# Kernel optimization log

Measured on AMD Instinct MI355X. Metric: run time of the kernel, lower is better.

Reference implementation:

```python
import jax, jax.numpy as jnp
import numpy as np

HIDDEN = 2048
NUM_HEADS = 16
HEAD = HIDDEN // NUM_HEADS  # 128
B, S = 4, 2048  # equal-length prefill sequences (cu_seqlens = arange(B+1)*S)


def setup_inputs() -> dict:
    key = jax.random.key(0)
    ks = jax.random.split(key, 5)
    return {
        "hidden_states": jax.random.normal(ks[0], (B * S, HIDDEN), jnp.float32),
        # fused QKV weight: rows ordered [q(all heads), k(all heads), v(all heads)]
        "w_qkv": jax.random.normal(ks[1], (3 * HIDDEN, HIDDEN), jnp.float32) * 0.02,
        "b_qkv": jax.random.normal(ks[2], (3 * HIDDEN,), jnp.float32) * 0.02,
        "w_dense": jax.random.normal(ks[3], (HIDDEN, HIDDEN), jnp.float32) * 0.02,
        "b_dense": jax.random.normal(ks[4], (HIDDEN,), jnp.float32) * 0.02,
        "batch_size": B,
        "seq_len": S,
    }


def reference(hidden_states, w_qkv, b_qkv, w_dense, b_dense, batch_size, seq_len):
    # QKV projection: [T, hidden] -> [T, 3, H, D]
    qkv = hidden_states @ w_qkv.T + b_qkv
    qkv = qkv.reshape(batch_size, seq_len, 3, NUM_HEADS, HEAD)
    q, k, v = qkv[:, :, 0], qkv[:, :, 1], qkv[:, :, 2]  # each [B, S, H, D]

    softmax_scale = HEAD ** -0.5
    # varlen causal flash attention (prefill path), per-sequence causal mask
    scores = jnp.einsum("bqhd,bkhd->bhqk", q, k) * softmax_scale
    causal = jnp.tril(jnp.ones((seq_len, seq_len), dtype=bool))
    scores = jnp.where(causal, scores, jnp.finfo(scores.dtype).min)
    probs = jax.nn.softmax(scores, axis=-1)
    attn = jnp.einsum("bhqk,bkhd->bqhd", probs, v)  # [B, S, H, D]

    attn = attn.reshape(batch_size * seq_len, NUM_HEADS * HEAD)
    # output projection (resid dropout p=0 -> identity)
    return attn @ w_dense.T + b_dense
```

## Files before the change

### kernel.cpp

```cpp
#include <hip/hip_runtime.h>
#include <hip/hip_bf16.h>

#define HIDDEN 2048
#define NHEADS 16
#define HEADD  128
#define BATCH  4
#define SEQ    2048
#define MROWS  (BATCH*SEQ)
#define NQKV   (3*HIDDEN)

typedef __attribute__((ext_vector_type(8))) short bf16x8;
typedef __attribute__((ext_vector_type(4))) float f32x4;

__device__ inline unsigned short f2bf(float f) {
  unsigned int u = __builtin_bit_cast(unsigned int, f);
  u += 0x7FFF + ((u >> 16) & 1);
  return (unsigned short)(u >> 16);
}

__device__ inline void async16(const void* g, void* s) {
  __builtin_amdgcn_global_load_lds(
      (__attribute__((address_space(1))) void*)(g),
      (__attribute__((address_space(3))) void*)(s), 16, 0, 0);
}

#define PH_BAR() asm volatile("s_barrier" ::: "memory")
#define LGKM0()  asm volatile("s_waitcnt lgkmcnt(0)" ::: "memory")
#define VMC6()   asm volatile("s_waitcnt vmcnt(6)" ::: "memory")
#define VMC0()   asm volatile("s_waitcnt vmcnt(0)" ::: "memory")

__global__ __launch_bounds__(256)
void cvt_f32_bf16(const float* __restrict__ in, unsigned short* __restrict__ out, int n) {
  int i = (blockIdx.x * 256 + threadIdx.x) * 8;
  if (i + 8 <= n) {
    float4 a = *(const float4*)&in[i];
    float4 b = *(const float4*)&in[i + 4];
    unsigned short o[8];
    o[0] = f2bf(a.x); o[1] = f2bf(a.y); o[2] = f2bf(a.z); o[3] = f2bf(a.w);
    o[4] = f2bf(b.x); o[5] = f2bf(b.y); o[6] = f2bf(b.z); o[7] = f2bf(b.w);
    *(uint4*)&out[i] = *(uint4*)o;
  }
}

#define MFMA_QUAD(AB, NB, AF, BF)                                           \
  _Pragma("unroll")                                                         \
  for (int mi = 0; mi < 4; ++mi)                                            \
    _Pragma("unroll")                                                       \
    for (int e = 0; e < 2; ++e)                                             \
      _Pragma("unroll")                                                     \
      for (int ks = 0; ks < 2; ++ks)                                        \
        acc[(AB) + mi][(NB) + e] = __builtin_amdgcn_mfma_f32_16x16x32_bf16( \
            AF[mi][ks], BF[e][ks], acc[(AB) + mi][(NB) + e], 0, 0, 0);

#define RD_A(DST, BUF, H)                                                   \
  _Pragma("unroll")                                                         \
  for (int mi = 0; mi < 4; ++mi) {                                          \
    DST[mi][0] = rdA(BUF, H, mi, 0);                                        \
    DST[mi][1] = rdA(BUF, H, mi, 1);                                        \
  }

#define RD_B(DST, BUF, H)                                                   \
  _Pragma("unroll")                                                         \
  for (int e = 0; e < 2; ++e) {                                             \
    DST[e][0] = rdB(BUF, H, e, 0);                                          \
    DST[e][1] = rdB(BUF, H, e, 1);                                          \
  }

template<int OUT_BF16>
__global__ __launch_bounds__(512, 2)
void gemm256(const unsigned short* __restrict__ A,
             const unsigned short* __restrict__ Bw,
             const float* __restrict__ bias,
             void* __restrict__ Cout, int M, int N, int K) {
  __shared__ __align__(16) unsigned short L[2][2][2][8192];

  const int t = threadIdx.x;
  const int lane = t & 63, wv = t >> 6;
  const int r = lane & 15, q = lane >> 4;
  const int wm = wv >> 2, wn = wv & 3;
  const int r7 = r & 7;

  const int gx = gridDim.x;
  const int nwg = gx * (int)gridDim.y;
  const int id = (int)blockIdx.y * gx + (int)blockIdx.x;
  const int swz = (id & 7) * (nwg >> 3) + (id >> 3);
  const int m0 = (swz / gx) * 256;
  const int n0 = (swz % gx) * 256;

  const int sub = t >> 3;
  const int cb = (t & 7) ^ (sub & 7);
  unsigned offA[2][2], offB[2][2];
#pragma unroll
  for (int ld = 0; ld < 2; ++ld) {
    int row = ld * 64 + sub;
    int fs = row >> 4, r16 = row & 15;
    int gA = (fs & 3) | ((fs >> 2) << 3);
    int gB = (fs & 1) | ((fs >> 1) << 2);
#pragma unroll
    for (int h = 0; h < 2; ++h) {
      offA[h][ld] = (unsigned)(m0 + (gA | (h << 2)) * 16 + r16) * (unsigned)K + cb * 8;
      offB[h][ld] = (unsigned)(n0 + (gB | (h << 1)) * 16 + r16) * (unsigned)K + cb * 8;
    }
  }

  auto stgA = [&](int buf, int h, int tile) {
    async16(A + (size_t)(offA[h][0] + (unsigned)tile * 64), &L[buf][0][h][t * 8]);
    async16(A + (size_t)(offA[h][1] + (unsigned)tile * 64), &L[buf][0][h][4096 + t * 8]);
  };
  auto stgB = [&](int buf, int h, int tile) {
    async16(Bw + (size_t)(offB[h][0] + (unsigned)tile * 64), &L[buf][1][h][t * 8]);
    async16(Bw + (size_t)(offB[h][1] + (unsigned)tile * 64), &L[buf][1][h][4096 + t * 8]);
  };
  auto rdA = [&](int buf, int h, int mi, int ks) -> bf16x8 {
    int row = (wm * 4 + mi) * 16 + r;
    int c = (ks * 4 + q) ^ r7;
    return *(const bf16x8*)&L[buf][0][h][row * 64 + c * 8];
  };
  auto rdB = [&](int buf, int h, int e, int ks) -> bf16x8 {
    int row = (wn * 2 + e) * 16 + r;
    int c = (ks * 4 + q) ^ r7;
    return *(const bf16x8*)&L[buf][1][h][row * 64 + c * 8];
  };

  f32x4 acc[8][4] = {};
  bf16x8 a0[4][2], a1[4][2], b0[2][2], b1[2][2];

  stgA(0, 0, 0); stgB(0, 0, 0); stgA(0, 1, 0); stgB(0, 1, 0);
  stgA(1, 0, 1); stgB(1, 0, 1); stgA(1, 1, 1);
  VMC6(); PH_BAR();

  const int NT = K >> 6;
  const int NITER = K >> 7;
#pragma unroll 1
  for (int i = 0; i < NITER; ++i) {
    const int ta = 2 * i + 1;
    int tb = 2 * i + 2; if (tb > NT - 1) tb = NT - 1;
    int tc = 2 * i + 3; if (tc > NT - 1) tc = NT - 1;

    RD_A(a0, 0, 0); RD_B(b0, 0, 0);
    stgB(1, 1, ta);
    PH_BAR(); LGKM0(); __builtin_amdgcn_s_setprio(1);
    MFMA_QUAD(0, 0, a0, b0);
    __builtin_amdgcn_s_setprio(0); PH_BAR();

    RD_A(a1, 0, 1);
    stgA(0, 0, tb);
    PH_BAR(); LGKM0(); __builtin_amdgcn_s_setprio(1);
    MFMA_QUAD(4, 0, a1, b0);
    __builtin_amdgcn_s_setprio(0); PH_BAR();

    RD_B(b1, 0, 1);
    stgB(0, 0, tb);
    PH_BAR(); LGKM0(); __builtin_amdgcn_s_setprio(1);
    MFMA_QUAD(4, 2, a1, b1);
    __builtin_amdgcn_s_setprio(0); PH_BAR();

    stgA(0, 1, tb);
    PH_BAR(); LGKM0(); __builtin_amdgcn_s_setprio(1);
    MFMA_QUAD(0, 2, a0, b1);
    __builtin_amdgcn_s_setprio(0); VMC6(); PH_BAR();

    RD_A(a0, 1, 0); RD_B(b0, 1, 0);
    stgB(0, 1, tb);
    PH_BAR(); LGKM0(); __builtin_amdgcn_s_setprio(1);
    MFMA_QUAD(0, 0, a0, b0);
    __builtin_amdgcn_s_setprio(0); PH_BAR();

    RD_A(a1, 1, 1);
    stgA(1, 0, tc);
    PH_BAR(); LGKM0(); __builtin_amdgcn_s_setprio(1);
    MFMA_QUAD(4, 0, a1, b0);
    __builtin_amdgcn_s_setprio(0); PH_BAR();

    RD_B(b1, 1, 1);
    stgB(1, 0, tc);
    PH_BAR(); LGKM0(); __builtin_amdgcn_s_setprio(1);
    MFMA_QUAD(4, 2, a1, b1);
    __builtin_amdgcn_s_setprio(0); PH_BAR();

    stgA(1, 1, tc);
    PH_BAR(); LGKM0(); __builtin_amdgcn_s_setprio(1);
    MFMA_QUAD(0, 2, a0, b1);
    __builtin_amdgcn_s_setprio(0); VMC6(); PH_BAR();
  }
  VMC0();

  float bv[4];
#pragma unroll
  for (int ni = 0; ni < 4; ++ni) bv[ni] = bias[n0 + (wn * 4 + ni) * 16 + r];
#pragma unroll
  for (int ai = 0; ai < 8; ++ai) {
    int grow = m0 + (wm * 8 + ai) * 16 + q * 4;
#pragma unroll
    for (int ni = 0; ni < 4; ++ni) {
      int gcol = n0 + (wn * 4 + ni) * 16 + r;
#pragma unroll
      for (int rr = 0; rr < 4; ++rr) {
        float v = acc[ai][ni][rr] + bv[ni];
        if (OUT_BF16)
          ((unsigned short*)Cout)[(size_t)(grow + rr) * N + gcol] = f2bf(v);
        else
          ((float*)Cout)[(size_t)(grow + rr) * N + gcol] = v;
      }
    }
  }
}

__global__ __launch_bounds__(256, 2)
void flash_attn(const unsigned short* __restrict__ qkv,
                unsigned short* __restrict__ attn,
                float* __restrict__ outP,
                float* __restrict__ lsumB)
{
  __shared__ __align__(16) unsigned short Ks[64][128];
  __shared__ __align__(16) unsigned short Vt[128][64];

  const int t = threadIdx.x;
  const int lane = t & 63, wv = t >> 6;
  const int r = lane & 15, q = lane >> 4;
  const int b = blockIdx.y >> 4, h = blockIdx.y & 15;

  int f = (int)blockIdx.x, qt, c;
  if (f < 8)       { qt = 15 - f; c = 0; }
  else if (f < 16) { qt = 23 - f; c = 1; }
  else             { qt = 23 - f; c = 0; }
  const int q0 = qt * 128;
  const int t0 = c * 16;
  int t1 = 2 * qt + 2; if (t1 > t0 + 16) t1 = t0 + 16;

  unsigned short* Ps = &Ks[0][0] + wv * 2048;

  const size_t rs = NQKV;
  const unsigned short* qbase = qkv + (size_t)(b * SEQ) * rs + h * HEADD;
  const unsigned short* kbase = qbase + HIDDEN;
  const unsigned short* vbase = qbase + 2 * HIDDEN;

  bf16x8 qf[2][4];
  for (int i = 0; i < 2; ++i)
    for (int ks = 0; ks < 4; ++ks)
      qf[i][ks] = *(const bf16x8*)(qbase +
          (size_t)(q0 + wv * 32 + i * 16 + r) * rs + ks * 32 + q * 8);

  f32x4 accO[2][8] = {};
  float lsum[2][4] = {};

  const int diag0 = 2 * qt;
  const float sc2 = 0.08838834764831845f * 1.4426950408889634f;

  const int koct = t & 15, krb = t >> 4;
  const int bd4 = t & 15, bkv4 = t >> 4;

  uint4 kreg[4], vreg[4];
  for (int s = 0; s < 4; ++s)
    kreg[s] = *(const uint4*)(kbase + (size_t)(t0 * 64 + krb + 16 * s) * rs + koct * 8);
  for (int jr = 0; jr < 4; ++jr)
    vreg[jr] = *(const uint4*)(vbase + (size_t)(t0 * 64 + bkv4 * 4 + jr) * rs + bd4 * 8);

  for (int tk = t0; tk < t1; ++tk) {
    LGKM0(); PH_BAR();
    for (int s = 0; s < 4; ++s) {
      int row = krb + 16 * s;
      int cbk = koct ^ (row & 7);
      *(uint4*)&Ks[row][cbk * 8] = kreg[s];
    }
    for (int jj = 0; jj < 8; ++jj) {
      int d = bd4 * 8 + jj;
      int cbk = (bkv4 >> 1) ^ jj ^ (bd4 & 7);
      unsigned short tmp[4];
      for (int jr = 0; jr < 4; ++jr)
        tmp[jr] = ((const unsigned short*)&vreg[jr])[jj];
      *(uint2*)&Vt[d][cbk * 8 + (bkv4 & 1) * 4] = *(const uint2*)tmp;
    }
    LGKM0(); PH_BAR();
    if (tk + 1 < t1) {
      for (int s = 0; s < 4; ++s)
        kreg[s] = *(const uint4*)(kbase + (size_t)((tk + 1) * 64 + krb + 16 * s) * rs + koct * 8);
      for (int jr = 0; jr < 4; ++jr)
        vreg[jr] = *(const uint4*)(vbase + (size_t)((tk + 1) * 64 + bkv4 * 4 + jr) * rs + bd4 * 8);
    }

    f32x4 s[2][4] = {};
    __builtin_amdgcn_s_setprio(1);
    for (int ks = 0; ks < 4; ++ks) {
      bf16x8 bk[4];
      for (int j = 0; j < 4; ++j) {
        int row = j * 16 + r;
        int cbk = (ks * 4 + q) ^ (r & 7);
        bk[j] = *(const bf16x8*)&Ks[row][cbk * 8];
      }
      for (int i = 0; i < 2; ++i)
        for (int j = 0; j < 4; ++j)
          s[i][j] = __builtin_amdgcn_mfma_f32_16x16x32_bf16(qf[i][ks], bk[j], s[i][j], 0, 0, 0);
    }
    __builtin_amdgcn_s_setprio(0);
    LGKM0(); PH_BAR();

    const bool diag = (tk >= diag0);
    for (int i = 0; i < 2; ++i) {
      float pvv[4][4];
      for (int j = 0; j < 4; ++j)
        for (int rr = 0; rr < 4; ++rr) {
          float v = s[i][j][rr] * sc2;
          if (diag) {
            int kvp = tk * 64 + j * 16 + r;
            int qp = q0 + wv * 32 + i * 16 + q * 4 + rr;
            if (kvp > qp) v = -1e30f;
          }
          float p = __builtin_amdgcn_exp2f(v);
          pvv[j][rr] = p;
          lsum[i][rr] += p;
        }
      for (int j = 0; j < 4; ++j)
        for (int rr = 0; rr < 4; ++rr) {
          int m = i * 16 + q * 4 + rr;
          int k = j * 16 + r;
          int cbk = (k >> 3) ^ (m & 7);
          Ps[m * 64 + cbk * 8 + (k & 7)] = f2bf(pvv[j][rr]);
        }
    }

    __builtin_amdgcn_s_setprio(1);
    for (int ks2 = 0; ks2 < 2; ++ks2) {
      bf16x8 ap[2];
      for (int i = 0; i < 2; ++i) {
        int m = i * 16 + r;
        int cbk = (ks2 * 4 + q) ^ (r & 7);
        ap[i] = *(const bf16x8*)&Ps[m * 64 + cbk * 8];
      }
      for (int n = 0; n < 8; ++n) {
        int dd = n * 16 + r;
        int cbk = (ks2 * 4 + q) ^ (r & 7) ^ ((n * 2 + (r >> 3)) & 7);
        bf16x8 bvv = *(const bf16x8*)&Vt[dd][cbk * 8];
        for (int i = 0; i < 2; ++i)
          accO[i][n] = __builtin_amdgcn_mfma_f32_16x16x32_bf16(ap[i], bvv, accO[i][n], 0, 0, 0);
      }
    }
    __builtin_amdgcn_s_setprio(0);
  }

  for (int i = 0; i < 2; ++i)
    for (int rr = 0; rr < 4; ++rr) {
      float l = lsum[i][rr];
      for (int off = 1; off < 16; off <<= 1)
        l += __shfl_xor(l, off, 64);
      lsum[i][rr] = l;
    }

  if (qt < 8) {
    for (int i = 0; i < 2; ++i)
      for (int rr = 0; rr < 4; ++rr) {
        int row = q0 + wv * 32 + i * 16 + q * 4 + rr;
        float inv = 1.0f / lsum[i][rr];
        size_t obase = (size_t)(b * SEQ + row) * HIDDEN + h * HEADD;
        for (int n = 0; n < 8; ++n)
          attn[obase + n * 16 + r] = f2bf(accO[i][n][rr] * inv);
      }
  } else {
    const int cb4 = c * 4 + b;
    for (int i = 0; i < 2; ++i)
      for (int rr = 0; rr < 4; ++rr) {
        int row = q0 + wv * 32 + i * 16 + q * 4 + rr;
        int rl = row - 1024;
        if (r == 0)
          lsumB[(size_t)(cb4 * 1024 + rl) * 16 + h] = lsum[i][rr];
        size_t obase = (size_t)(cb4 * 1024 + rl) * 2048 + h * HEADD;
        for (int n = 0; n < 8; ++n)
          outP[obase + n * 16 + r] = accO[i][n][rr];
      }
  }
}

__global__ __launch_bounds__(256)
void attn_norm(const float* __restrict__ outP, const float* __restrict__ lsumB,
               unsigned short* __restrict__ attn) {
  size_t j = ((size_t)blockIdx.x * 256 + threadIdx.x) * 8;
  int b = (int)(j >> 21);
  int rl = (int)(j >> 11) & 1023;
  int col = (int)j & 2047;
  int h = col >> 7;
  float l = lsumB[(size_t)(b * 1024 + rl) * 16 + h]
          + lsumB[(size_t)((4 + b) * 1024 + rl) * 16 + h];
  float inv = 1.0f / l;
  size_t p0 = (size_t)(b * 1024 + rl) * 2048 + col;
  size_t p1 = p0 + (size_t)4 * 1024 * 2048;
  float4 a0 = *(const float4*)&outP[p0];
  float4 a1 = *(const float4*)&outP[p0 + 4];
  float4 c0 = *(const float4*)&outP[p1];
  float4 c1 = *(const float4*)&outP[p1 + 4];
  unsigned short o[8];
  o[0] = f2bf((a0.x + c0.x) * inv); o[1] = f2bf((a0.y + c0.y) * inv);
  o[2] = f2bf((a0.z + c0.z) * inv); o[3] = f2bf((a0.w + c0.w) * inv);
  o[4] = f2bf((a1.x + c1.x) * inv); o[5] = f2bf((a1.y + c1.y) * inv);
  o[6] = f2bf((a1.z + c1.z) * inv); o[7] = f2bf((a1.w + c1.w) * inv);
  size_t base = (size_t)(b * 2048 + 1024 + rl) * 2048 + col;
  *(uint4*)&attn[base] = *(uint4*)o;
}

extern "C" void kernel_launch(void* const* d_in, const int* in_sizes, int n_in,
                              void* d_out, int out_size, void* d_ws, size_t ws_size,
                              hipStream_t stream) {
  const float* hs      = (const float*)d_in[0];
  const float* w_qkv   = (const float*)d_in[1];
  const float* b_qkv   = (const float*)d_in[2];
  const float* w_dense = (const float*)d_in[3];
  const float* b_dense = (const float*)d_in[4];

  char* ws = (char*)d_ws;
  unsigned short* hsb  = (unsigned short*)ws;
  unsigned short* wqb  = (unsigned short*)(ws + 33554432);
  unsigned short* qkvb = (unsigned short*)(ws + 33554432 + 25165824);
  unsigned short* attnb = hsb;
  unsigned short* wdb   = wqb;
  float* lsumB = (float*)(ws + 33554432 + 16777216);
  float* outP  = (float*)d_out;

  cvt_f32_bf16<<<MROWS * HIDDEN / 2048, 256, 0, stream>>>(hs, hsb, MROWS * HIDDEN);
  cvt_f32_bf16<<<NQKV * HIDDEN / 2048, 256, 0, stream>>>(w_qkv, wqb, NQKV * HIDDEN);

  gemm256<1><<<dim3(NQKV / 256, MROWS / 256), 512, 0, stream>>>(
      hsb, wqb, b_qkv, qkvb, MROWS, NQKV, HIDDEN);

  flash_attn<<<dim3(24, BATCH * NHEADS), 256, 0, stream>>>(qkvb, attnb, outP, lsumB);

  cvt_f32_bf16<<<HIDDEN * HIDDEN / 2048, 256, 0, stream>>>(w_dense, wdb, HIDDEN * HIDDEN);

  attn_norm<<<4096, 256, 0, stream>>>(outP, lsumB, attnb);

  gemm256<0><<<dim3(HIDDEN / 256, MROWS / 256), 512, 0, stream>>>(
      attnb, wdb, b_dense, d_out, MROWS, HIDDEN, HIDDEN);
}
```

Before: 614.2 us.

## Split flash attention query tile across eight waves of 16 rows each

The attention block goes from 256 to 512 threads. Each wave now owns 16 query rows instead of 32, and K/V staging is spread over twice as many threads with half the registers per thread. The aim is to cut per-wave register pressure so more waves fit per CU and latency is better hidden. In exchange, each loaded K/V tile is reused by fewer MFMAs per wave, and barriers now synchronise more waves.

Result: slower. 650.0 us (+5.8%).

```diff
diff --git a/kernel.cpp b/kernel.cpp
--- a/kernel.cpp
+++ b/kernel.cpp
@@ -206,7 +206,7 @@
   }
 }
 
-__global__ __launch_bounds__(256, 2)
+__global__ __launch_bounds__(512, 4)
 void flash_attn(const unsigned short* __restrict__ qkv,
                 unsigned short* __restrict__ attn,
                 float* __restrict__ outP,
@@ -225,24 +225,23 @@
   else if (f < 16) { qt = 23 - f; c = 1; }
   else             { qt = 23 - f; c = 0; }
   const int q0 = qt * 128;
-  const int t0 = c * 16;
-  int t1 = 2 * qt + 2; if (t1 > t0 + 16) t1 = t0 + 16;
-
-  unsigned short* Ps = &Ks[0][0] + wv * 2048;
+  const int t0c = c * 16;
+  int t1 = 2 * qt + 2; if (t1 > t0c + 16) t1 = t0c + 16;
+
+  unsigned short* Ps = &Ks[0][0] + wv * 1024;
 
   const size_t rs = NQKV;
   const unsigned short* qbase = qkv + (size_t)(b * SEQ) * rs + h * HEADD;
   const unsigned short* kbase = qbase + HIDDEN;
   const unsigned short* vbase = qbase + 2 * HIDDEN;
 
-  bf16x8 qf[2][4];
-  for (int i = 0; i < 2; ++i)
-    for (int ks = 0; ks < 4; ++ks)
-      qf[i][ks] = *(const bf16x8*)(qbase +
-          (size_t)(q0 + wv * 32 + i * 16 + r) * rs + ks * 32 + q * 8);
-
-  f32x4 accO[2][8] = {};
-  float lsum[2][4] = {};
+  bf16x8 qf[4];
+  for (int ks = 0; ks < 4; ++ks)
+    qf[ks] = *(const bf16x8*)(qbase +
+        (size_t)(q0 + wv * 16 + r) * rs + ks * 32 + q * 8);
+
+  f32x4 accO[8] = {};
+  float lsum[4] = {};
 
   const int diag0 = 2 * qt;
   const float sc2 = 0.08838834764831845f * 1.4426950408889634f;
@@ -250,36 +249,36 @@
   const int koct = t & 15, krb = t >> 4;
   const int bd4 = t & 15, bkv4 = t >> 4;
 
-  uint4 kreg[4], vreg[4];
-  for (int s = 0; s < 4; ++s)
-    kreg[s] = *(const uint4*)(kbase + (size_t)(t0 * 64 + krb + 16 * s) * rs + koct * 8);
-  for (int jr = 0; jr < 4; ++jr)
-    vreg[jr] = *(const uint4*)(vbase + (size_t)(t0 * 64 + bkv4 * 4 + jr) * rs + bd4 * 8);
-
-  for (int tk = t0; tk < t1; ++tk) {
+  uint4 kreg[2], vreg[2];
+  for (int s = 0; s < 2; ++s)
+    kreg[s] = *(const uint4*)(kbase + (size_t)(t0c * 64 + krb + 32 * s) * rs + koct * 8);
+  for (int jr = 0; jr < 2; ++jr)
+    vreg[jr] = *(const uint4*)(vbase + (size_t)(t0c * 64 + bkv4 * 2 + jr) * rs + bd4 * 8);
+
+  for (int tk = t0c; tk < t1; ++tk) {
     LGKM0(); PH_BAR();
-    for (int s = 0; s < 4; ++s) {
-      int row = krb + 16 * s;
+    for (int s = 0; s < 2; ++s) {
+      int row = krb + 32 * s;
       int cbk = koct ^ (row & 7);
       *(uint4*)&Ks[row][cbk * 8] = kreg[s];
     }
     for (int jj = 0; jj < 8; ++jj) {
       int d = bd4 * 8 + jj;
-      int cbk = (bkv4 >> 1) ^ jj ^ (bd4 & 7);
-      unsigned short tmp[4];
-      for (int jr = 0; jr < 4; ++jr)
-        tmp[jr] = ((const unsigned short*)&vreg[jr])[jj];
-      *(uint2*)&Vt[d][cbk * 8 + (bkv4 & 1) * 4] = *(const uint2*)tmp;
+      int cbk = (bkv4 >> 2) ^ jj ^ (bd4 & 7);
+      unsigned short tmp2[2];
+      tmp2[0] = ((const unsigned short*)&vreg[0])[jj];
+      tmp2[1] = ((const unsigned short*)&vreg[1])[jj];
+      *(unsigned int*)&Vt[d][cbk * 8 + (bkv4 & 3) * 2] = *(const unsigned int*)tmp2;
     }
     LGKM0(); PH_BAR();
     if (tk + 1 < t1) {
-      for (int s = 0; s < 4; ++s)
-        kreg[s] = *(const uint4*)(kbase + (size_t)((tk + 1) * 64 + krb + 16 * s) * rs + koct * 8);
-      for (int jr = 0; jr < 4; ++jr)
-        vreg[jr] = *(const uint4*)(vbase + (size_t)((tk + 1) * 64 + bkv4 * 4 + jr) * rs + bd4 * 8);
-    }
-
-    f32x4 s[2][4] = {};
+      for (int s = 0; s < 2; ++s)
+        kreg[s] = *(const uint4*)(kbase + (size_t)((tk + 1) * 64 + krb + 32 * s) * rs + koct * 8);
+      for (int jr = 0; jr < 2; ++jr)
+        vreg[jr] = *(const uint4*)(vbase + (size_t)((tk + 1) * 64 + bkv4 * 2 + jr) * rs + bd4 * 8);
+    }
+
+    f32x4 s4[4] = {};
     __builtin_amdgcn_s_setprio(1);
     for (int ks = 0; ks < 4; ++ks) {
       bf16x8 bk[4];
@@ -288,85 +287,69 @@
         int cbk = (ks * 4 + q) ^ (r & 7);
         bk[j] = *(const bf16x8*)&Ks[row][cbk * 8];
       }
-      for (int i = 0; i < 2; ++i)
-        for (int j = 0; j < 4; ++j)
-          s[i][j] = __builtin_amdgcn_mfma_f32_16x16x32_bf16(qf[i][ks], bk[j], s[i][j], 0, 0, 0);
+      for (int j = 0; j < 4; ++j)
+        s4[j] = __builtin_amdgcn_mfma_f32_16x16x32_bf16(qf[ks], bk[j], s4[j], 0, 0, 0);
     }
     __builtin_amdgcn_s_setprio(0);
     LGKM0(); PH_BAR();
 
     const bool diag = (tk >= diag0);
-    for (int i = 0; i < 2; ++i) {
-      float pvv[4][4];
-      for (int j = 0; j < 4; ++j)
-        for (int rr = 0; rr < 4; ++rr) {
-          float v = s[i][j][rr] * sc2;
-          if (diag) {
-            int kvp = tk * 64 + j * 16 + r;
-            int qp = q0 + wv * 32 + i * 16 + q * 4 + rr;
-            if (kvp > qp) v = -1e30f;
-          }
-          float p = __builtin_amdgcn_exp2f(v);
-          pvv[j][rr] = p;
-          lsum[i][rr] += p;
+    for (int j = 0; j < 4; ++j)
+      for (int rr = 0; rr < 4; ++rr) {
+        float v = s4[j][rr] * sc2;
+        if (diag) {
+          int kvp = tk * 64 + j * 16 + r;
+          int qp = q0 + wv * 16 + q * 4 + rr;
+          if (kvp > qp) v = -1e30f;
         }
-      for (int j = 0; j < 4; ++j)
-        for (int rr = 0; rr < 4; ++rr) {
-          int m = i * 16 + q * 4 + rr;
-          int k = j * 16 + r;
-          int cbk = (k >> 3) ^ (m & 7);
-          Ps[m * 64 + cbk * 8 + (k & 7)] = f2bf(pvv[j][rr]);
-        }
-    }
+        float p = __builtin_amdgcn_exp2f(v);
+        lsum[rr] += p;
+        int m = q * 4 + rr;
+        int k = j * 16 + r;
+        int cbk = (k >> 3) ^ (m & 7);
+        Ps[m * 64 + cbk * 8 + (k & 7)] = f2bf(p);
+      }
 
     __builtin_amdgcn_s_setprio(1);
     for (int ks2 = 0; ks2 < 2; ++ks2) {
-      bf16x8 ap[2];
-      for (int i = 0; i < 2; ++i) {
-        int m = i * 16 + r;
-        int cbk = (ks2 * 4 + q) ^ (r & 7);
-        ap[i] = *(const bf16x8*)&Ps[m * 64 + cbk * 8];
-      }
+      int cba = (ks2 * 4 + q) ^ (r & 7);
+      bf16x8 ap = *(const bf16x8*)&Ps[r * 64 + cba * 8];
       for (int n = 0; n < 8; ++n) {
         int dd = n * 16 + r;
         int cbk = (ks2 * 4 + q) ^ (r & 7) ^ ((n * 2 + (r >> 3)) & 7);
         bf16x8 bvv = *(const bf16x8*)&Vt[dd][cbk * 8];
-        for (int i = 0; i < 2; ++i)
-          accO[i][n] = __builtin_amdgcn_mfma_f32_16x16x32_bf16(ap[i], bvv, accO[i][n], 0, 0, 0);
+        accO[n] = __builtin_amdgcn_mfma_f32_16x16x32_bf16(ap, bvv, accO[n], 0, 0, 0);
       }
     }
     __builtin_amdgcn_s_setprio(0);
   }
 
-  for (int i = 0; i < 2; ++i)
+  for (int rr = 0; rr < 4; ++rr) {
+    float l = lsum[rr];
+    for (int off = 1; off < 16; off <<= 1)
+      l += __shfl_xor(l, off, 64);
+    lsum[rr] = l;
+  }
+
+  if (qt < 8) {
     for (int rr = 0; rr < 4; ++rr) {
-      float l = lsum[i][rr];
-      for (int off = 1; off < 16; off <<= 1)
-        l += __shfl_xor(l, off, 64);
-      lsum[i][rr] = l;
-    }
-
-  if (qt < 8) {
-    for (int i = 0; i < 2; ++i)
-      for (int rr = 0; rr < 4; ++rr) {
-        int row = q0 + wv * 32 + i * 16 + q * 4 + rr;
-        float inv = 1.0f / lsum[i][rr];
-        size_t obase = (size_t)(b * SEQ + row) * HIDDEN + h * HEADD;
-        for (int n = 0; n < 8; ++n)
-          attn[obase + n * 16 + r] = f2bf(accO[i][n][rr] * inv);
-      }
+      int row = q0 + wv * 16 + q * 4 + rr;
+      float inv = 1.0f / lsum[rr];
+      size_t obase = (size_t)(b * SEQ + row) * HIDDEN + h * HEADD;
+      for (int n = 0; n < 8; ++n)
+        attn[obase + n * 16 + r] = f2bf(accO[n][rr] * inv);
+    }
   } else {
     const int cb4 = c * 4 + b;
-    for (int i = 0; i < 2; ++i)
-      for (int rr = 0; rr < 4; ++rr) {
-        int row = q0 + wv * 32 + i * 16 + q * 4 + rr;
-        int rl = row - 1024;
-        if (r == 0)
-          lsumB[(size_t)(cb4 * 1024 + rl) * 16 + h] = lsum[i][rr];
-        size_t obase = (size_t)(cb4 * 1024 + rl) * 2048 + h * HEADD;
-        for (int n = 0; n < 8; ++n)
-          outP[obase + n * 16 + r] = accO[i][n][rr];
-      }
+    for (int rr = 0; rr < 4; ++rr) {
+      int row = q0 + wv * 16 + q * 4 + rr;
+      int rl = row - 1024;
+      if (r == 0)
+        lsumB[(size_t)(cb4 * 1024 + rl) * 16 + h] = lsum[rr];
+      size_t obase = (size_t)(cb4 * 1024 + rl) * 2048 + h * HEADD;
+      for (int n = 0; n < 8; ++n)
+        outP[obase + n * 16 + r] = accO[n][rr];
+    }
   }
 }
 
@@ -420,7 +403,7 @@
   gemm256<1><<<dim3(NQKV / 256, MROWS / 256), 512, 0, stream>>>(
       hsb, wqb, b_qkv, qkvb, MROWS, NQKV, HIDDEN);
 
-  flash_attn<<<dim3(24, BATCH * NHEADS), 256, 0, stream>>>(qkvb, attnb, outP, lsumB);
+  flash_attn<<<dim3(24, BATCH * NHEADS), 512, 0, stream>>>(qkvb, attnb, outP, lsumB);
 
   cvt_f32_bf16<<<HIDDEN * HIDDEN / 2048, 256, 0, stream>>>(w_dense, wdb, HIDDEN * HIDDEN);
 
```
